# Performance work log

Hardware: AMD Instinct MI355X
Metric: run time of the kernel (lower is better)

The kernel has to match this reference:

```python
import jax, jax.numpy as jnp
import numpy as np
import math

B, S, DIM = 2, 2048, 1024
H, D = 16, 64  # num_head, head_dim; H*D == DIM

def setup_inputs() -> dict:
    key = jax.random.key(0)
    ks = jax.random.split(key, 10)
    s = 0.02
    return {
        "X": jax.random.normal(ks[0], (B, S, DIM), dtype=jnp.float32),
        "mask": jnp.ones((B, S), dtype=jnp.float32),
        "Wq": jax.random.normal(ks[1], (DIM, H * D), dtype=jnp.float32) * s,
        "bq": jnp.zeros((H * D,), dtype=jnp.float32),
        "Wk": jax.random.normal(ks[2], (DIM, H * D), dtype=jnp.float32) * s,
        "bk": jnp.zeros((H * D,), dtype=jnp.float32),
        "Wv": jax.random.normal(ks[3], (DIM, H * D), dtype=jnp.float32) * s,
        "bv": jnp.zeros((H * D,), dtype=jnp.float32),
        "Wo": jax.random.normal(ks[4], (H * D, DIM), dtype=jnp.float32) * s,
        "bo": jnp.zeros((DIM,), dtype=jnp.float32),
    }

def _split_heads(x):
    # [B, S, H*D] -> [B, H, S, D]
    b, s, _ = x.shape
    return x.reshape(b, s, H, D).transpose(0, 2, 1, 3)

def reference(X, mask, Wq, bq, Wk, bk, Wv, bv, Wo, bo):
    Q = _split_heads(X @ Wq + bq)
    K = _split_heads(X @ Wk + bk)
    V = _split_heads(X @ Wv + bv)
    # scaled dot-product attention with additive mask penalty
    dot = jnp.einsum('bhqd,bhkd->bhqk', Q, K) / math.sqrt(D)
    dot = dot - 1e6 * (1.0 - mask[:, None, None, :])
    attn = jax.nn.softmax(dot, axis=-1)
    ctx = jnp.einsum('bhqk,bhkd->bhqd', attn, V)
    # combine heads: [B, H, S, D] -> [B, S, H*D]
    ctx = ctx.transpose(0, 2, 1, 3).reshape(B, S, H * D)
    return ctx @ Wo + bo
```

## Files before the change

kernel.cpp:

```cpp
#include <hip/hip_runtime.h>
#include <cstdint>
#include <cstddef>

typedef __attribute__((ext_vector_type(8))) _Float16 f16x8;
typedef __attribute__((ext_vector_type(4))) _Float16 f16x4;
typedef __attribute__((ext_vector_type(4))) float f32x4;

#define MFMA_16x16x32(a, b, c) __builtin_amdgcn_mfma_f32_16x16x32_f16((a), (b), (c), 0, 0, 0)
#define MFMA_16x16x16(a, b, c) __builtin_amdgcn_mfma_f32_16x16x16f16((a), (b), (c), 0, 0, 0)

static constexpr int kB = 2, kS = 2048, kDim = 1024, kH = 16, kD = 64;
static constexpr int kM = kB * kS;
static constexpr float kQScale = 0.125f * 1.44269504088896340736f;
static constexpr float kPenC = 1.44269504088896340736e6f;

__device__ __forceinline__ void wg_barrier_lds() {
  asm volatile("s_waitcnt lgkmcnt(0)" ::: "memory");
  __builtin_amdgcn_s_barrier();
}

__global__ void cvt_f32_to_f16(const float* __restrict__ in, _Float16* __restrict__ out, int n8) {
  int i = blockIdx.x * blockDim.x + threadIdx.x;
  if (i >= n8) return;
  const float4* p = (const float4*)in + (size_t)i * 2;
  float4 a = p[0], b = p[1];
  f16x8 h;
  h[0] = (_Float16)a.x; h[1] = (_Float16)a.y; h[2] = (_Float16)a.z; h[3] = (_Float16)a.w;
  h[4] = (_Float16)b.x; h[5] = (_Float16)b.y; h[6] = (_Float16)b.z; h[7] = (_Float16)b.w;
  ((f16x8*)out)[i] = h;
}

__global__ void transpose_cvt_w(const float* __restrict__ w0, const float* __restrict__ w1,
                                const float* __restrict__ w2, const float* __restrict__ w3,
                                _Float16* __restrict__ o0, _Float16* __restrict__ o1,
                                _Float16* __restrict__ o2, _Float16* __restrict__ o3) {
  const float* w; _Float16* o;
  switch (blockIdx.z) {
    case 0: w = w0; o = o0; break;
    case 1: w = w1; o = o1; break;
    case 2: w = w2; o = o2; break;
    default: w = w3; o = o3; break;
  }
  __shared__ alignas(16) _Float16 tile[64][72];
  const int kt = blockIdx.x * 64;
  const int nt = blockIdx.y * 64;
  const int tr = threadIdx.x >> 4;
  const int tc = threadIdx.x & 15;
#pragma unroll
  for (int rr = 0; rr < 4; ++rr) {
    int r = rr * 16 + tr;
    float4 v = *(const float4*)&w[(size_t)(kt + r) * kDim + nt + tc * 4];
    f16x4 hv;
    hv[0] = (_Float16)v.x; hv[1] = (_Float16)v.y; hv[2] = (_Float16)v.z; hv[3] = (_Float16)v.w;
    *(f16x4*)&tile[r][tc * 4] = hv;
  }
  __syncthreads();
#pragma unroll
  for (int rr = 0; rr < 4; ++rr) {
    int nl = rr * 16 + tr;
    f16x4 hv;
    hv[0] = tile[tc * 4 + 0][nl];
    hv[1] = tile[tc * 4 + 1][nl];
    hv[2] = tile[tc * 4 + 2][nl];
    hv[3] = tile[tc * 4 + 3][nl];
    *(f16x4*)&o[(size_t)(nt + nl) * kDim + kt + tc * 4] = hv;
  }
}

__global__ __launch_bounds__(256, 2) void gemm_qkv(
    const _Float16* __restrict__ A,
    const _Float16* __restrict__ wt0, const _Float16* __restrict__ wt1, const _Float16* __restrict__ wt2,
    const float* __restrict__ bias0, const float* __restrict__ bias1, const float* __restrict__ bias2,
    _Float16* __restrict__ oq, _Float16* __restrict__ ok, _Float16* __restrict__ ov) {
  const _Float16* Bt; const float* bias; _Float16* out;
  switch (blockIdx.z) {
    case 0: Bt = wt0; bias = bias0; out = oq; break;
    case 1: Bt = wt1; bias = bias1; out = ok; break;
    default: Bt = wt2; bias = bias2; out = ov; break;
  }
  __shared__ alignas(16) _Float16 As[2][128 * 72];
  __shared__ alignas(16) _Float16 Bs[2][128 * 72];
  const int tid = threadIdx.x;
  const int lane = tid & 63;
  const int wave = tid >> 6;
  const int wm = wave & 1, wn = wave >> 1;
  const int l15 = lane & 15, quad = lane >> 4;
  const int m0 = blockIdx.x * 128, n0 = blockIdx.y * 128;

  const int srow = tid >> 3;
  const int skc = (tid & 7) * 8;

  f32x4 acc[4][4] = {};
  f16x8 ra[4], rb[4];

#pragma unroll
  for (int i = 0; i < 4; ++i) {
    int row = srow + 32 * i;
    ra[i] = *(const f16x8*)&A[(size_t)(m0 + row) * kDim + skc];
    rb[i] = *(const f16x8*)&Bt[(size_t)(n0 + row) * kDim + skc];
  }
#pragma unroll
  for (int i = 0; i < 4; ++i) {
    int row = srow + 32 * i;
    *(f16x8*)&As[0][row * 72 + skc] = ra[i];
    *(f16x8*)&Bs[0][row * 72 + skc] = rb[i];
  }

  for (int kt = 0; kt < 16; ++kt) {
    const int cur = kt & 1;
    if (kt + 1 < 16) {
      int k0 = (kt + 1) * 64;
#pragma unroll
      for (int i = 0; i < 4; ++i) {
        int row = srow + 32 * i;
        ra[i] = *(const f16x8*)&A[(size_t)(m0 + row) * kDim + k0 + skc];
        rb[i] = *(const f16x8*)&Bt[(size_t)(n0 + row) * kDim + k0 + skc];
      }
    }
    wg_barrier_lds();
#pragma unroll
    for (int kk = 0; kk < 2; ++kk) {
      f16x8 af[4], bf[4];
#pragma unroll
      for (int t = 0; t < 4; ++t) af[t] = *(const f16x8*)&As[cur][(wm * 64 + t * 16 + l15) * 72 + kk * 32 + quad * 8];
#pragma unroll
      for (int t = 0; t < 4; ++t) bf[t] = *(const f16x8*)&Bs[cur][(wn * 64 + t * 16 + l15) * 72 + kk * 32 + quad * 8];
      __builtin_amdgcn_s_setprio(1);
#pragma unroll
      for (int i = 0; i < 4; ++i)
#pragma unroll
        for (int j = 0; j < 4; ++j)
          acc[i][j] = MFMA_16x16x32(af[i], bf[j], acc[i][j]);
      __builtin_amdgcn_s_setprio(0);
    }
    if (kt + 1 < 16) {
#pragma unroll
      for (int i = 0; i < 4; ++i) {
        int row = srow + 32 * i;
        *(f16x8*)&As[cur ^ 1][row * 72 + skc] = ra[i];
        *(f16x8*)&Bs[cur ^ 1][row * 72 + skc] = rb[i];
      }
    }
  }

  const int mbase = m0 + wm * 64 + quad * 4;
  const int nbase = n0 + wn * 64 + l15;
  if (blockIdx.z == 2) {
#pragma unroll
    for (int j = 0; j < 4; ++j) {
      int n = nbase + j * 16;
      float bv = bias[n];
      int h = n >> 6, d = n & 63;
#pragma unroll
      for (int i = 0; i < 4; ++i) {
        int m = mbase + i * 16;
        int b = m >> 11, s = m & (kS - 1);
        f16x4 hv;
#pragma unroll
        for (int r = 0; r < 4; ++r) hv[r] = (_Float16)(acc[i][j][r] + bv);
        *(f16x4*)&out[((size_t)((b * kH + h) * kD + d)) * kS + s] = hv;
      }
    }
  } else {
    const float osc = (blockIdx.z == 0) ? kQScale : 1.0f;
#pragma unroll
    for (int j = 0; j < 4; ++j) {
      int n = nbase + j * 16;
      float bv = bias[n];
      int h = n >> 6, d = n & 63;
#pragma unroll
      for (int i = 0; i < 4; ++i) {
        int mrow = mbase + i * 16;
#pragma unroll
        for (int r = 0; r < 4; ++r) {
          int m = mrow + r;
          int b = m >> 11, s = m & (kS - 1);
          out[(size_t)(((b * kH + h) * kS) + s) * kD + d] = (_Float16)((acc[i][j][r] + bv) * osc);
        }
      }
    }
  }
}

__global__ __launch_bounds__(256, 2) void attn(
    const _Float16* __restrict__ Q, const _Float16* __restrict__ K,
    const _Float16* __restrict__ V, const float* __restrict__ mask,
    _Float16* __restrict__ ctx) {
  const int id = blockIdx.x;
  const int logical = (id & 7) * 64 + (id >> 3);
  const int bh = logical >> 4;
  const int qblk = logical & 15;
  const int b = bh >> 4;
  const int q0 = qblk * 128;
  const int tid = threadIdx.x, lane = tid & 63, wave = tid >> 6;
  const int l15 = lane & 15, quad = lane >> 4;

  __shared__ alignas(16) _Float16 Ks[2][128 * 72];
  __shared__ alignas(16) _Float16 Vs[2][64 * 136];
  __shared__ alignas(16) float pens[kS];

  const _Float16* Qh = Q + (size_t)bh * kS * kD;
  const _Float16* Kh = K + (size_t)bh * kS * kD;
  const _Float16* Vh = V + (size_t)bh * kS * kD;

#pragma unroll
  for (int i = 0; i < 2; ++i) {
    float4 mv4 = *(const float4*)&mask[(size_t)b * kS + tid * 8 + i * 4];
    float4 pv;
    pv.x = (mv4.x - 1.0f) * kPenC;
    pv.y = (mv4.y - 1.0f) * kPenC;
    pv.z = (mv4.z - 1.0f) * kPenC;
    pv.w = (mv4.w - 1.0f) * kPenC;
    *(float4*)&pens[tid * 8 + i * 4] = pv;
  }

  f16x8 qf[2][2];
#pragma unroll
  for (int t = 0; t < 2; ++t) {
    int qrow = q0 + wave * 32 + t * 16 + l15;
#pragma unroll
    for (int kk = 0; kk < 2; ++kk)
      qf[t][kk] = *(const f16x8*)&Qh[(size_t)qrow * kD + kk * 32 + quad * 8];
  }

  f16x4 ones4;
#pragma unroll
  for (int i = 0; i < 4; ++i) ones4[i] = (_Float16)1.0f;

  f32x4 o_acc[2][4] = {};
  f32x4 l_acc[2] = {};

  const int srow = tid >> 3;
  const int skc = (tid & 7) * 8;
  const int vrow = tid >> 4;
  const int vcol = (tid & 15) * 8;

  f16x8 kreg[4], vreg[4];
#pragma unroll
  for (int i = 0; i < 4; ++i)
    kreg[i] = *(const f16x8*)&Kh[(size_t)(srow + 32 * i) * kD + skc];
#pragma unroll
  for (int i = 0; i < 4; ++i)
    vreg[i] = *(const f16x8*)&Vh[(size_t)(vrow + 16 * i) * kS + vcol];
#pragma unroll
  for (int i = 0; i < 4; ++i)
    *(f16x8*)&Ks[0][(srow + 32 * i) * 72 + skc] = kreg[i];
#pragma unroll
  for (int i = 0; i < 4; ++i)
    *(f16x8*)&Vs[0][(vrow + 16 * i) * 136 + vcol] = vreg[i];

  for (int it = 0; it < 16; ++it) {
    const int cur = it & 1;
    const int kb = it * 128;
    if (it + 1 < 16) {
#pragma unroll
      for (int i = 0; i < 4; ++i)
        kreg[i] = *(const f16x8*)&Kh[(size_t)(kb + 128 + srow + 32 * i) * kD + skc];
#pragma unroll
      for (int i = 0; i < 4; ++i)
        vreg[i] = *(const f16x8*)&Vh[(size_t)(vrow + 16 * i) * kS + kb + 128 + vcol];
    }
    wg_barrier_lds();

#pragma unroll
    for (int colt = 0; colt < 8; ++colt) {
      f16x8 kf0 = *(const f16x8*)&Ks[cur][(colt * 16 + l15) * 72 + quad * 8];
      f16x8 kf1 = *(const f16x8*)&Ks[cur][(colt * 16 + l15) * 72 + 32 + quad * 8];
      f32x4 s0 = {}, s1 = {};
      __builtin_amdgcn_s_setprio(1);
      s0 = MFMA_16x16x32(kf0, qf[0][0], s0);
      s0 = MFMA_16x16x32(kf1, qf[0][1], s0);
      s1 = MFMA_16x16x32(kf0, qf[1][0], s1);
      s1 = MFMA_16x16x32(kf1, qf[1][1], s1);
      __builtin_amdgcn_s_setprio(0);
      f32x4 pn = *(const f32x4*)&pens[kb + colt * 16 + quad * 4];
      f16x4 pa0, pa1;
#pragma unroll
      for (int r = 0; r < 4; ++r) {
        pa0[r] = (_Float16)__builtin_exp2f(s0[r] + pn[r]);
        pa1[r] = (_Float16)__builtin_exp2f(s1[r] + pn[r]);
      }
      f16x4 vf0 = *(const f16x4*)&Vs[cur][(0 * 16 + l15) * 136 + colt * 16 + quad * 4];
      f16x4 vf1 = *(const f16x4*)&Vs[cur][(1 * 16 + l15) * 136 + colt * 16 + quad * 4];
      f16x4 vf2 = *(const f16x4*)&Vs[cur][(2 * 16 + l15) * 136 + colt * 16 + quad * 4];
      f16x4 vf3 = *(const f16x4*)&Vs[cur][(3 * 16 + l15) * 136 + colt * 16 + quad * 4];
      __builtin_amdgcn_s_setprio(1);
      o_acc[0][0] = MFMA_16x16x16(pa0, vf0, o_acc[0][0]);
      o_acc[0][1] = MFMA_16x16x16(pa0, vf1, o_acc[0][1]);
      o_acc[0][2] = MFMA_16x16x16(pa0, vf2, o_acc[0][2]);
      o_acc[0][3] = MFMA_16x16x16(pa0, vf3, o_acc[0][3]);
      o_acc[1][0] = MFMA_16x16x16(pa1, vf0, o_acc[1][0]);
      o_acc[1][1] = MFMA_16x16x16(pa1, vf1, o_acc[1][1]);
      o_acc[1][2] = MFMA_16x16x16(pa1, vf2, o_acc[1][2]);
      o_acc[1][3] = MFMA_16x16x16(pa1, vf3, o_acc[1][3]);
      l_acc[0] = MFMA_16x16x16(pa0, ones4, l_acc[0]);
      l_acc[1] = MFMA_16x16x16(pa1, ones4, l_acc[1]);
      __builtin_amdgcn_s_setprio(0);
    }

    if (it + 1 < 16) {
#pragma unroll
      for (int i = 0; i < 4; ++i)
        *(f16x8*)&Ks[cur ^ 1][(srow + 32 * i) * 72 + skc] = kreg[i];
#pragma unroll
      for (int i = 0; i < 4; ++i)
        *(f16x8*)&Vs[cur ^ 1][(vrow + 16 * i) * 136 + vcol] = vreg[i];
    }
  }

  const int h = bh & 15;
#pragma unroll
  for (int t = 0; t < 2; ++t) {
    f32x4 linv;
#pragma unroll
    for (int r = 0; r < 4; ++r) linv[r] = 1.0f / l_acc[t][r];
    int qbase = q0 + wave * 32 + t * 16 + quad * 4;
#pragma unroll
    for (int c = 0; c < 4; ++c) {
#pragma unroll
      for (int r = 0; r < 4; ++r) {
        ctx[((size_t)(b * kS + qbase + r)) * kDim + h * kD + c * 16 + l15] =
            (_Float16)(o_acc[t][c][r] * linv[r]);
      }
    }
  }
}

__global__ __launch_bounds__(256, 2) void gemm_out(
    const _Float16* __restrict__ A, const _Float16* __restrict__ Bt,
    const float* __restrict__ bias, float* __restrict__ out) {
  __shared__ alignas(16) _Float16 As[2][64 * 72];
  __shared__ alignas(16) _Float16 Bs[2][128 * 72];
  const int tid = threadIdx.x;
  const int lane = tid & 63;
  const int wave = tid >> 6;
  const int wm = wave & 1, wn = wave >> 1;
  const int l15 = lane & 15, quad = lane >> 4;
  const int m0 = blockIdx.x * 64, n0 = blockIdx.y * 128;

  const int srow = tid >> 3;
  const int skc = (tid & 7) * 8;

  f32x4 acc[2][4] = {};
  f16x8 ra[2], rb[4];

#pragma unroll
  for (int i = 0; i < 2; ++i)
    ra[i] = *(const f16x8*)&A[(size_t)(m0 + srow + 32 * i) * kDim + skc];
#pragma unroll
  for (int i = 0; i < 4; ++i)
    rb[i] = *(const f16x8*)&Bt[(size_t)(n0 + srow + 32 * i) * kDim + skc];
#pragma unroll
  for (int i = 0; i < 2; ++i)
    *(f16x8*)&As[0][(srow + 32 * i) * 72 + skc] = ra[i];
#pragma unroll
  for (int i = 0; i < 4; ++i)
    *(f16x8*)&Bs[0][(srow + 32 * i) * 72 + skc] = rb[i];

  for (int kt = 0; kt < 16; ++kt) {
    const int cur = kt & 1;
    if (kt + 1 < 16) {
      int k0 = (kt + 1) * 64;
#pragma unroll
      for (int i = 0; i < 2; ++i)
        ra[i] = *(const f16x8*)&A[(size_t)(m0 + srow + 32 * i) * kDim + k0 + skc];
#pragma unroll
      for (int i = 0; i < 4; ++i)
        rb[i] = *(const f16x8*)&Bt[(size_t)(n0 + srow + 32 * i) * kDim + k0 + skc];
    }
    wg_barrier_lds();
#pragma unroll
    for (int kk = 0; kk < 2; ++kk) {
      f16x8 af[2], bf[4];
#pragma unroll
      for (int t = 0; t < 2; ++t) af[t] = *(const f16x8*)&As[cur][(wm * 32 + t * 16 + l15) * 72 + kk * 32 + quad * 8];
#pragma unroll
      for (int t = 0; t < 4; ++t) bf[t] = *(const f16x8*)&Bs[cur][(wn * 64 + t * 16 + l15) * 72 + kk * 32 + quad * 8];
      __builtin_amdgcn_s_setprio(1);
#pragma unroll
      for (int i = 0; i < 2; ++i)
#pragma unroll
        for (int j = 0; j < 4; ++j)
          acc[i][j] = MFMA_16x16x32(af[i], bf[j], acc[i][j]);
      __builtin_amdgcn_s_setprio(0);
    }
    if (kt + 1 < 16) {
#pragma unroll
      for (int i = 0; i < 2; ++i)
        *(f16x8*)&As[cur ^ 1][(srow + 32 * i) * 72 + skc] = ra[i];
#pragma unroll
      for (int i = 0; i < 4; ++i)
        *(f16x8*)&Bs[cur ^ 1][(srow + 32 * i) * 72 + skc] = rb[i];
    }
  }

  const int mbase = m0 + wm * 32 + quad * 4;
  const int nbase = n0 + wn * 64 + l15;
#pragma unroll
  for (int j = 0; j < 4; ++j) {
    int n = nbase + j * 16;
    float bv = bias[n];
#pragma unroll
    for (int i = 0; i < 2; ++i) {
      int mrow = mbase + i * 16;
#pragma unroll
      for (int r = 0; r < 4; ++r)
        out[(size_t)(mrow + r) * kDim + n] = acc[i][j][r] + bv;
    }
  }
}

extern "C" void kernel_launch(void* const* d_in, const int* in_sizes, int n_in,
                              void* d_out, int out_size, void* d_ws, size_t ws_size,
                              hipStream_t stream) {
  (void)in_sizes; (void)n_in; (void)out_size; (void)ws_size;
  const float* X    = (const float*)d_in[0];
  const float* mask = (const float*)d_in[1];
  const float* Wq   = (const float*)d_in[2];
  const float* bq   = (const float*)d_in[3];
  const float* Wk   = (const float*)d_in[4];
  const float* bk   = (const float*)d_in[5];
  const float* Wv   = (const float*)d_in[6];
  const float* bv   = (const float*)d_in[7];
  const float* Wo   = (const float*)d_in[8];
  const float* bo   = (const float*)d_in[9];
  float* out = (float*)d_out;

  char* ws = (char*)d_ws;
  _Float16* Xh   = (_Float16*)(ws);
  _Float16* Wqt  = (_Float16*)(ws + ((size_t)8  << 20));
  _Float16* Wkt  = (_Float16*)(ws + ((size_t)10 << 20));
  _Float16* Wvt  = (_Float16*)(ws + ((size_t)12 << 20));
  _Float16* Wot  = (_Float16*)(ws + ((size_t)14 << 20));
  _Float16* Qh   = (_Float16*)(ws + ((size_t)16 << 20));
  _Float16* Kh   = (_Float16*)(ws + ((size_t)24 << 20));
  _Float16* Vh   = (_Float16*)(ws + ((size_t)32 << 20));
  _Float16* Ch   = (_Float16*)(ws + ((size_t)40 << 20));

  cvt_f32_to_f16<<<dim3(kM * kDim / 8 / 256), dim3(256), 0, stream>>>(X, Xh, kM * kDim / 8);
  transpose_cvt_w<<<dim3(16, 16, 4), dim3(256), 0, stream>>>(Wq, Wk, Wv, Wo, Wqt, Wkt, Wvt, Wot);
  gemm_qkv<<<dim3(32, 8, 3), dim3(256), 0, stream>>>(Xh, Wqt, Wkt, Wvt, bq, bk, bv, Qh, Kh, Vh);
  attn<<<dim3(512), dim3(256), 0, stream>>>(Qh, Kh, Vh, mask, Ch);
  gemm_out<<<dim3(64, 8), dim3(256), 0, stream>>>(Ch, Wot, bo, out);
}
```

Baseline: 205.3 us.

## Split attention key range across two wave groups with LDS reduction

The attention kernel now launches 512 threads per block: eight waves split into four query strips and two key groups. Each step loads a 256-key chunk into both LDS buffers, and each key group processes its own 128-key half. Partial O and l accumulators are then summed through LDS at the end. The mask penalty is also folded into the MFMA accumulator init, which removes an add per element. This aims to double the waves in flight for latency hiding, at the cost of an extra barrier per step, a final reduction, and loads that are no longer overlapped with compute in the same way.

```diff
diff --git a/kernel.cpp b/kernel.cpp
--- a/kernel.cpp
+++ b/kernel.cpp
@@ -182,7 +182,7 @@
   }
 }
 
-__global__ __launch_bounds__(256, 2) void attn(
+__global__ __launch_bounds__(512, 4) void attn(
     const _Float16* __restrict__ Q, const _Float16* __restrict__ K,
     const _Float16* __restrict__ V, const float* __restrict__ mask,
     _Float16* __restrict__ ctx) {
@@ -193,6 +193,8 @@
   const int b = bh >> 4;
   const int q0 = qblk * 128;
   const int tid = threadIdx.x, lane = tid & 63, wave = tid >> 6;
+  const int strip = wave & 3;
+  const int kgrp = wave >> 2;
   const int l15 = lane & 15, quad = lane >> 4;
 
   __shared__ alignas(16) _Float16 Ks[2][128 * 72];
@@ -203,21 +205,20 @@
   const _Float16* Kh = K + (size_t)bh * kS * kD;
   const _Float16* Vh = V + (size_t)bh * kS * kD;
 
-#pragma unroll
-  for (int i = 0; i < 2; ++i) {
-    float4 mv4 = *(const float4*)&mask[(size_t)b * kS + tid * 8 + i * 4];
+  {
+    float4 mv4 = *(const float4*)&mask[(size_t)b * kS + tid * 4];
     float4 pv;
     pv.x = (mv4.x - 1.0f) * kPenC;
     pv.y = (mv4.y - 1.0f) * kPenC;
     pv.z = (mv4.z - 1.0f) * kPenC;
     pv.w = (mv4.w - 1.0f) * kPenC;
-    *(float4*)&pens[tid * 8 + i * 4] = pv;
+    *(float4*)&pens[tid * 4] = pv;
   }
 
   f16x8 qf[2][2];
 #pragma unroll
   for (int t = 0; t < 2; ++t) {
-    int qrow = q0 + wave * 32 + t * 16 + l15;
+    int qrow = q0 + strip * 32 + t * 16 + l15;
 #pragma unroll
     for (int kk = 0; kk < 2; ++kk)
       qf[t][kk] = *(const f16x8*)&Qh[(size_t)qrow * kD + kk * 32 + quad * 8];
@@ -230,60 +231,68 @@
   f32x4 o_acc[2][4] = {};
   f32x4 l_acc[2] = {};
 
-  const int srow = tid >> 3;
   const int skc = (tid & 7) * 8;
-  const int vrow = tid >> 4;
   const int vcol = (tid & 15) * 8;
 
   f16x8 kreg[4], vreg[4];
 #pragma unroll
-  for (int i = 0; i < 4; ++i)
-    kreg[i] = *(const f16x8*)&Kh[(size_t)(srow + 32 * i) * kD + skc];
-#pragma unroll
-  for (int i = 0; i < 4; ++i)
-    vreg[i] = *(const f16x8*)&Vh[(size_t)(vrow + 16 * i) * kS + vcol];
-#pragma unroll
-  for (int i = 0; i < 4; ++i)
-    *(f16x8*)&Ks[0][(srow + 32 * i) * 72 + skc] = kreg[i];
-#pragma unroll
-  for (int i = 0; i < 4; ++i)
-    *(f16x8*)&Vs[0][(vrow + 16 * i) * 136 + vcol] = vreg[i];
-
-  for (int it = 0; it < 16; ++it) {
-    const int cur = it & 1;
-    const int kb = it * 128;
-    if (it + 1 < 16) {
-#pragma unroll
-      for (int i = 0; i < 4; ++i)
-        kreg[i] = *(const f16x8*)&Kh[(size_t)(kb + 128 + srow + 32 * i) * kD + skc];
-#pragma unroll
-      for (int i = 0; i < 4; ++i)
-        vreg[i] = *(const f16x8*)&Vh[(size_t)(vrow + 16 * i) * kS + kb + 128 + vcol];
-    }
+  for (int i = 0; i < 4; ++i) {
+    int rr = (tid >> 3) + 64 * i;
+    kreg[i] = *(const f16x8*)&Kh[(size_t)rr * kD + skc];
+  }
+#pragma unroll
+  for (int i = 0; i < 4; ++i) {
+    int vrr = (tid >> 4) + 32 * i;
+    vreg[i] = *(const f16x8*)&Vh[(size_t)(vrr & 63) * kS + (vrr >> 6) * 128 + vcol];
+  }
+#pragma unroll
+  for (int i = 0; i < 4; ++i) {
+    int rr = (tid >> 3) + 64 * i;
+    *(f16x8*)&Ks[rr >> 7][(rr & 127) * 72 + skc] = kreg[i];
+  }
+#pragma unroll
+  for (int i = 0; i < 4; ++i) {
+    int vrr = (tid >> 4) + 32 * i;
+    *(f16x8*)&Vs[vrr >> 6][(vrr & 63) * 136 + vcol] = vreg[i];
+  }
+
+  for (int s = 0; s < 8; ++s) {
     wg_barrier_lds();
-
+    if (s + 1 < 8) {
+      int nb = (s + 1) * 256;
+#pragma unroll
+      for (int i = 0; i < 4; ++i) {
+        int rr = (tid >> 3) + 64 * i;
+        kreg[i] = *(const f16x8*)&Kh[(size_t)(nb + rr) * kD + skc];
+      }
+#pragma unroll
+      for (int i = 0; i < 4; ++i) {
+        int vrr = (tid >> 4) + 32 * i;
+        vreg[i] = *(const f16x8*)&Vh[(size_t)(vrr & 63) * kS + nb + (vrr >> 6) * 128 + vcol];
+      }
+    }
+
+    const int kb = s * 256 + kgrp * 128;
 #pragma unroll
     for (int colt = 0; colt < 8; ++colt) {
-      f16x8 kf0 = *(const f16x8*)&Ks[cur][(colt * 16 + l15) * 72 + quad * 8];
-      f16x8 kf1 = *(const f16x8*)&Ks[cur][(colt * 16 + l15) * 72 + 32 + quad * 8];
-      f32x4 s0 = {}, s1 = {};
-      __builtin_amdgcn_s_setprio(1);
+      f32x4 pn = *(const f32x4*)&pens[kb + colt * 16 + quad * 4];
+      f16x8 kf0 = *(const f16x8*)&Ks[kgrp][(colt * 16 + l15) * 72 + quad * 8];
+      f16x8 kf1 = *(const f16x8*)&Ks[kgrp][(colt * 16 + l15) * 72 + 32 + quad * 8];
+      f32x4 s0 = pn, s1 = pn;
       s0 = MFMA_16x16x32(kf0, qf[0][0], s0);
       s0 = MFMA_16x16x32(kf1, qf[0][1], s0);
       s1 = MFMA_16x16x32(kf0, qf[1][0], s1);
       s1 = MFMA_16x16x32(kf1, qf[1][1], s1);
-      __builtin_amdgcn_s_setprio(0);
-      f32x4 pn = *(const f32x4*)&pens[kb + colt * 16 + quad * 4];
+      f16x4 vf0 = *(const f16x4*)&Vs[kgrp][(0 * 16 + l15) * 136 + colt * 16 + quad * 4];
+      f16x4 vf1 = *(const f16x4*)&Vs[kgrp][(1 * 16 + l15) * 136 + colt * 16 + quad * 4];
+      f16x4 vf2 = *(const f16x4*)&Vs[kgrp][(2 * 16 + l15) * 136 + colt * 16 + quad * 4];
+      f16x4 vf3 = *(const f16x4*)&Vs[kgrp][(3 * 16 + l15) * 136 + colt * 16 + quad * 4];
       f16x4 pa0, pa1;
 #pragma unroll
       for (int r = 0; r < 4; ++r) {
-        pa0[r] = (_Float16)__builtin_exp2f(s0[r] + pn[r]);
-        pa1[r] = (_Float16)__builtin_exp2f(s1[r] + pn[r]);
-      }
-      f16x4 vf0 = *(const f16x4*)&Vs[cur][(0 * 16 + l15) * 136 + colt * 16 + quad * 4];
-      f16x4 vf1 = *(const f16x4*)&Vs[cur][(1 * 16 + l15) * 136 + colt * 16 + quad * 4];
-      f16x4 vf2 = *(const f16x4*)&Vs[cur][(2 * 16 + l15) * 136 + colt * 16 + quad * 4];
-      f16x4 vf3 = *(const f16x4*)&Vs[cur][(3 * 16 + l15) * 136 + colt * 16 + quad * 4];
+        pa0[r] = (_Float16)__builtin_exp2f(s0[r]);
+        pa1[r] = (_Float16)__builtin_exp2f(s1[r]);
+      }
       __builtin_amdgcn_s_setprio(1);
       o_acc[0][0] = MFMA_16x16x16(pa0, vf0, o_acc[0][0]);
       o_acc[0][1] = MFMA_16x16x16(pa0, vf1, o_acc[0][1]);
@@ -298,29 +307,50 @@
       __builtin_amdgcn_s_setprio(0);
     }
 
-    if (it + 1 < 16) {
-#pragma unroll
-      for (int i = 0; i < 4; ++i)
-        *(f16x8*)&Ks[cur ^ 1][(srow + 32 * i) * 72 + skc] = kreg[i];
-#pragma unroll
-      for (int i = 0; i < 4; ++i)
-        *(f16x8*)&Vs[cur ^ 1][(vrow + 16 * i) * 136 + vcol] = vreg[i];
-    }
-  }
-
-  const int h = bh & 15;
-#pragma unroll
-  for (int t = 0; t < 2; ++t) {
-    f32x4 linv;
-#pragma unroll
-    for (int r = 0; r < 4; ++r) linv[r] = 1.0f / l_acc[t][r];
-    int qbase = q0 + wave * 32 + t * 16 + quad * 4;
-#pragma unroll
-    for (int c = 0; c < 4; ++c) {
-#pragma unroll
-      for (int r = 0; r < 4; ++r) {
-        ctx[((size_t)(b * kS + qbase + r)) * kDim + h * kD + c * 16 + l15] =
-            (_Float16)(o_acc[t][c][r] * linv[r]);
+    wg_barrier_lds();
+    if (s + 1 < 8) {
+#pragma unroll
+      for (int i = 0; i < 4; ++i) {
+        int rr = (tid >> 3) + 64 * i;
+        *(f16x8*)&Ks[rr >> 7][(rr & 127) * 72 + skc] = kreg[i];
+      }
+#pragma unroll
+      for (int i = 0; i < 4; ++i) {
+        int vrr = (tid >> 4) + 32 * i;
+        *(f16x8*)&Vs[vrr >> 6][(vrr & 63) * 136 + vcol] = vreg[i];
+      }
+    }
+  }
+
+  f32x4* obuf = (f32x4*)&Ks[0][0];
+  f32x4* lbuf = (f32x4*)&Vs[0][0];
+  if (kgrp == 1) {
+#pragma unroll
+    for (int t = 0; t < 2; ++t) {
+#pragma unroll
+      for (int c = 0; c < 4; ++c)
+        obuf[(((strip * 2 + t) * 4 + c) << 6) + lane] = o_acc[t][c];
+      lbuf[((strip * 2 + t) << 6) + lane] = l_acc[t];
+    }
+  }
+  wg_barrier_lds();
+  if (kgrp == 0) {
+    const int h = bh & 15;
+#pragma unroll
+    for (int t = 0; t < 2; ++t) {
+      f32x4 lsum = l_acc[t] + lbuf[((strip * 2 + t) << 6) + lane];
+      f32x4 linv;
+#pragma unroll
+      for (int r = 0; r < 4; ++r) linv[r] = 1.0f / lsum[r];
+      int qbase = q0 + strip * 32 + t * 16 + quad * 4;
+#pragma unroll
+      for (int c = 0; c < 4; ++c) {
+        f32x4 o = o_acc[t][c] + obuf[(((strip * 2 + t) * 4 + c) << 6) + lane];
+#pragma unroll
+        for (int r = 0; r < 4; ++r) {
+          ctx[((size_t)(b * kS + qbase + r)) * kDim + h * kD + c * 16 + l15] =
+              (_Float16)(o[r] * linv[r]);
+        }
       }
     }
   }
@@ -440,6 +470,6 @@
   cvt_f32_to_f16<<<dim3(kM * kDim / 8 / 256), dim3(256), 0, stream>>>(X, Xh, kM * kDim / 8);
   transpose_cvt_w<<<dim3(16, 16, 4), dim3(256), 0, stream>>>(Wq, Wk, Wv, Wo, Wqt, Wkt, Wvt, Wot);
   gemm_qkv<<<dim3(32, 8, 3), dim3(256), 0, stream>>>(Xh, Wqt, Wkt, Wvt, bq, bk, bv, Qh, Kh, Vh);
-  attn<<<dim3(512), dim3(256), 0, stream>>>(Qh, Kh, Vh, mask, Ch);
+  attn<<<dim3(512), dim3(512), 0, stream>>>(Qh, Kh, Vh, mask, Ch);
   gemm_out<<<dim3(64, 8), dim3(256), 0, stream>>>(Ch, Wot, bo, out);
 }
```

Result: no change. 206.9 us (+0.8%).
